# Kernel tuning notes

Measured on AMD Instinct MI355X. Metric: run time of the kernel, lower is better.

Reference implementation:

```python
import jax, jax.numpy as jnp
import numpy as np
from jax import lax

IMG_SIZE = 512
STRIDE = 16
NUM_ANCHORS = 5
NUM_CLASSES = 80
TOPK = 1000
CONF_THRESH = 0.05
NMS_THRESH = 0.6
ANCHOR_SIZE = [[32, 32], [64, 64], [128, 96], [96, 128], [256, 256]]
B = 32
FMP = IMG_SIZE // STRIDE          # 32
M = FMP * FMP * NUM_ANCHORS       # 5120


def _make_anchors():
    # mirrors YOWO.generate_anchors: grid xy (in pixels) + per-cell anchor wh
    ys, xs = jnp.meshgrid(jnp.arange(FMP), jnp.arange(FMP), indexing='ij')
    xy = jnp.stack([xs, ys], axis=-1).astype(jnp.float32).reshape(-1, 2)   # [HW,2]
    xy = jnp.repeat(xy[:, None, :], NUM_ANCHORS, axis=1) * STRIDE          # [HW,A,2]
    wh = jnp.broadcast_to(jnp.asarray(ANCHOR_SIZE, jnp.float32)[None],
                          (FMP * FMP, NUM_ANCHORS, 2))                     # [HW,A,2]
    return jnp.concatenate([xy, wh], axis=-1).reshape(-1, 4)               # [M,4]


def setup_inputs() -> dict:
    key = jax.random.key(0)
    k1, k2, k3 = jax.random.split(key, 3)
    return {
        'conf_pred': jax.random.normal(k1, (B, M, 1), jnp.float32),
        'cls_pred': jax.random.normal(k2, (B, M, NUM_CLASSES), jnp.float32),
        'reg_pred': jax.random.normal(k3, (B, M, 4), jnp.float32),
        'anchor_boxes': _make_anchors(),
    }


def _decode_bbox(anchors, reg_pred):
    # anchors/reg_pred: [..., 4] -> xyxy boxes in pixels
    xy = jax.nn.sigmoid(reg_pred[..., :2]) * STRIDE + anchors[..., :2]
    wh = jnp.exp(reg_pred[..., 2:]) * anchors[..., 2:]
    return jnp.concatenate([xy - 0.5 * wh, xy + 0.5 * wh], axis=-1)


def _pairwise_iou(boxes):
    # boxes: [K,4] xyxy -> [K,K] IoU with the exact epsilons of YOWO.nms
    x1, y1, x2, y2 = boxes[:, 0], boxes[:, 1], boxes[:, 2], boxes[:, 3]
    areas = (x2 - x1) * (y2 - y1)
    xx1 = jnp.maximum(x1[:, None], x1[None, :])
    yy1 = jnp.maximum(y1[:, None], y1[None, :])
    xx2 = jnp.minimum(x2[:, None], x2[None, :])
    yy2 = jnp.minimum(y2[:, None], y2[None, :])
    w = jnp.maximum(1e-28, xx2 - xx1)
    h = jnp.maximum(1e-28, yy2 - yy1)
    inter = w * h
    return inter / (areas[:, None] + areas[None, :] - inter + 1e-14)


def _sequential_nms_keep(iou):
    # boxes assumed sorted by descending score; greedy sequential suppression
    K = iou.shape[0]
    idx = jnp.arange(K)

    def body(i, keep):
        sup = (iou[i] > NMS_THRESH) & (idx > i) & keep[i]
        return keep & ~sup

    return lax.fori_loop(0, K, body, jnp.ones(K, bool))


def reference(conf_pred, cls_pred, reg_pred, anchor_boxes):
    # scoring: sigmoid(obj) * softmax(cls), max over classes  -> [B,M]
    score_all = jax.nn.sigmoid(conf_pred) * jax.nn.softmax(cls_pred, axis=-1)
    scores = jnp.max(score_all, axis=-1)
    labels = jnp.argmax(score_all, axis=-1)

    # topk (lax.top_k returns scores sorted descending)  -> [B,TOPK]
    scores, idx = lax.top_k(scores, TOPK)
    labels = jnp.take_along_axis(labels, idx, axis=1)
    reg_sel = jnp.take_along_axis(reg_pred, idx[..., None], axis=1)
    anc_sel = anchor_boxes[idx]                                   # [B,TOPK,4]

    bboxes = jnp.clip(_decode_bbox(anc_sel, reg_sel) / IMG_SIZE, 0.0, 1.0)

    # per-class NMS via class-offset trick (boxes in [0,1], offset 2.0 per class)
    boxes_off = bboxes + 2.0 * labels.astype(bboxes.dtype)[..., None]
    iou = jax.vmap(_pairwise_iou)(boxes_off)                      # [B,TOPK,TOPK]
    nms_keep = jax.vmap(_sequential_nms_keep)(iou)                # [B,TOPK] bool

    keep = nms_keep & (scores >= CONF_THRESH)
    scores_out = jnp.where(keep, scores, 0.0)
    return scores_out, labels, bboxes, keep
```

## Files before the change

kernel.cpp:

```cpp
#include <hip/hip_runtime.h>
#include <cstdint>
#include <math.h>

constexpr int B = 32;
constexpr int M = 5120;
constexpr int C = 80;
constexpr int K = 1000;
constexpr float NMS_T  = 0.6f;

constexpr int OFF_SCORE = 0;
constexpr int OFF_LAB   = B * K;
constexpr int OFF_BOX   = 2 * B * K;
constexpr int OFF_KEEP  = 2 * B * K + 4 * B * K;

constexpr size_t WS_KEYS     = 0;
constexpr size_t WS_LABELS   = WS_KEYS   + (size_t)B * M * 8;
constexpr size_t WS_SELIDX   = WS_LABELS + (size_t)B * M * 4;
constexpr size_t WS_SELSC    = WS_SELIDX + (size_t)B * K * 4;
constexpr size_t WS_SELLAB   = WS_SELSC + (size_t)B * K * 4;
constexpr size_t WS_BOXOFF   = WS_SELLAB + (size_t)B * K * 4;
constexpr size_t WS_MASK     = WS_BOXOFF + (size_t)B * K * 4 * 4;

__device__ __forceinline__ float expf_cr(float x) {
    return (float)exp((double)x);
}
__device__ __forceinline__ float sigm_np(float x) {
    float e = expf_cr(-x);
    return __fdiv_rn(1.0f, __fadd_rn(1.0f, e));
}

__global__ void k_scores(const float* __restrict__ conf, const float* __restrict__ cls,
                         unsigned long long* __restrict__ keys, int* __restrict__ labels) {
    int m = blockIdx.x * blockDim.x + threadIdx.x;
    int b = blockIdx.y;
    size_t t = (size_t)b * M + m;
    const float4* rowv = (const float4*)(cls + t * C);
    float ev[80];
#pragma unroll
    for (int i = 0; i < 20; i++) {
        float4 v = rowv[i];
        ev[4 * i + 0] = v.x; ev[4 * i + 1] = v.y;
        ev[4 * i + 2] = v.z; ev[4 * i + 3] = v.w;
    }
    float mx = ev[0];
#pragma unroll
    for (int c = 1; c < 80; c++) mx = fmaxf(mx, ev[c]);
#pragma unroll
    for (int c = 0; c < 80; c++) ev[c] = expf_cr(__fsub_rn(ev[c], mx));
    float r[8];
#pragma unroll
    for (int j = 0; j < 8; j++) r[j] = ev[j];
#pragma unroll
    for (int i = 8; i < 80; i += 8)
#pragma unroll
        for (int j = 0; j < 8; j++) r[j] = __fadd_rn(r[j], ev[i + j]);
    float sum = __fadd_rn(
        __fadd_rn(__fadd_rn(r[0], r[1]), __fadd_rn(r[2], r[3])),
        __fadd_rn(__fadd_rn(r[4], r[5]), __fadd_rn(r[6], r[7])));
    float s = sigm_np(conf[t]);
    float best = -1.0f; int bi = 0;
#pragma unroll
    for (int c = 0; c < 80; c++) {
        float p  = __fdiv_rn(ev[c], sum);
        float sc = __fmul_rn(s, p);
        if (sc > best) { best = sc; bi = c; }
    }
    keys[t] = ((unsigned long long)__float_as_uint(best) << 32) |
              (unsigned long long)(0xFFFFFFFFu - (unsigned)m);
    labels[t] = bi;
}

__global__ void __launch_bounds__(1024)
k_topk(const unsigned long long* __restrict__ keys,
       const int* __restrict__ labels,
       int* __restrict__ sel_idx, float* __restrict__ sel_score,
       int* __restrict__ sel_label) {
    int b = blockIdx.x;
    int tid = threadIdx.x;
    const unsigned long long* kb = keys + (size_t)b * M;

    __shared__ unsigned int hist[2048];
    __shared__ unsigned int sufA[2048];
    __shared__ unsigned int sufB[2048];
    __shared__ unsigned long long cand[2048];
    __shared__ int scnt, thrBin, ovf;

    for (int i = tid; i < 2048; i += 1024) hist[i] = 0;
    if (tid == 0) { scnt = 0; ovf = 0; }
    __syncthreads();

    unsigned long long k5[5];
#pragma unroll
    for (int i = 0; i < 5; i++) {
        k5[i] = kb[tid + i * 1024];
        atomicAdd(&hist[(unsigned)(k5[i] >> 51)], 1u);
    }
    __syncthreads();
    for (int i = tid; i < 2048; i += 1024) sufA[i] = hist[i];
    __syncthreads();
    unsigned int* src = sufA; unsigned int* dst = sufB;
    for (int d = 1; d < 2048; d <<= 1) {
        for (int i = tid; i < 2048; i += 1024) {
            unsigned int v = src[i];
            if (i + d < 2048) v += src[i + d];
            dst[i] = v;
        }
        __syncthreads();
        unsigned int* tmp = src; src = dst; dst = tmp;
    }
    for (int i = tid; i < 2048; i += 1024) {
        unsigned int s = src[i];
        unsigned int sn = (i + 1 < 2048) ? src[i + 1] : 0u;
        if (s >= (unsigned)K && sn < (unsigned)K) thrBin = i;
    }
    __syncthreads();
    int T = thrBin;
#pragma unroll
    for (int i = 0; i < 5; i++) {
        if ((int)(k5[i] >> 51) >= T) {
            int pos = atomicAdd(&scnt, 1);
            if (pos < 2048) cand[pos] = k5[i]; else ovf = 1;
        }
    }
    __syncthreads();
    if (!ovf) {
        int S = scnt;
        for (int i = tid; i < 2048; i += 1024)
            if (i >= S) cand[i] = 0ull;
        __syncthreads();
        for (int ksz = 2; ksz <= 2048; ksz <<= 1) {
            for (int jsz = ksz >> 1; jsz > 0; jsz >>= 1) {
                int i = 2 * tid - (tid & (jsz - 1));
                unsigned long long a = cand[i], c = cand[i + jsz];
                bool desc = ((i & ksz) == 0);
                if ((a < c) == desc) { cand[i] = c; cand[i + jsz] = a; }
                __syncthreads();
            }
        }
        if (tid < K) {
            unsigned long long key = cand[tid];
            unsigned int mm = 0xFFFFFFFFu - (unsigned)(key & 0xFFFFFFFFu);
            sel_idx[b * K + tid] = (int)mm;
            sel_score[b * K + tid] = __uint_as_float((unsigned)(key >> 32));
            sel_label[b * K + tid] = labels[(size_t)b * M + mm];
        }
    } else {
#pragma unroll
        for (int i = 0; i < 5; i++) {
            unsigned long long my = k5[i];
            int rank = 0;
            for (int j = 0; j < M; j++) rank += (kb[j] > my) ? 1 : 0;
            if (rank < K) {
                int mm = tid + i * 1024;
                sel_idx[b * K + rank] = mm;
                sel_score[b * K + rank] = __uint_as_float((unsigned)(my >> 32));
                sel_label[b * K + rank] = labels[(size_t)b * M + mm];
            }
        }
    }
}

__global__ void k_decode(const float* __restrict__ reg, const float* __restrict__ anchors,
                         const int* __restrict__ sel_idx, const int* __restrict__ sel_label,
                         float* __restrict__ out, float4* __restrict__ boxes_off) {
    int k = blockIdx.x * blockDim.x + threadIdx.x;
    int b = blockIdx.y;
    if (k >= K) return;
    int m = sel_idx[b * K + k];
    float4 r = ((const float4*)reg)[(size_t)b * M + m];
    float4 a = ((const float4*)anchors)[m];
    float cx = __fadd_rn(__fmul_rn(sigm_np(r.x), 16.0f), a.x);
    float cy = __fadd_rn(__fmul_rn(sigm_np(r.y), 16.0f), a.y);
    float w  = __fmul_rn(expf_cr(r.z), a.z);
    float h  = __fmul_rn(expf_cr(r.w), a.w);
    float x1 = __fdiv_rn(__fsub_rn(cx, __fmul_rn(0.5f, w)), 512.0f);
    float y1 = __fdiv_rn(__fsub_rn(cy, __fmul_rn(0.5f, h)), 512.0f);
    float x2 = __fdiv_rn(__fadd_rn(cx, __fmul_rn(0.5f, w)), 512.0f);
    float y2 = __fdiv_rn(__fadd_rn(cy, __fmul_rn(0.5f, h)), 512.0f);
    x1 = fminf(fmaxf(x1, 0.0f), 1.0f);
    y1 = fminf(fmaxf(y1, 0.0f), 1.0f);
    x2 = fminf(fmaxf(x2, 0.0f), 1.0f);
    y2 = fminf(fmaxf(y2, 0.0f), 1.0f);
    int lab = sel_label[b * K + k];
    ((float4*)(out + OFF_BOX))[b * K + k] = make_float4(x1, y1, x2, y2);
    out[OFF_LAB + b * K + k] = (float)lab;
    float off = __fmul_rn(2.0f, (float)lab);
    boxes_off[b * K + k] = make_float4(__fadd_rn(x1, off), __fadd_rn(y1, off),
                                       __fadd_rn(x2, off), __fadd_rn(y2, off));
}

__global__ void __launch_bounds__(256)
k_mask(const float4* __restrict__ boxes_off,
       unsigned long long* __restrict__ mask) {
    int b = blockIdx.z;
    int rowTile = blockIdx.x;
    int wgGroup = blockIdx.y;
    int tid = threadIdx.x;
    __shared__ float4 sbj[256];
    __shared__ float  saj[256];
    __shared__ float4 sbi[64];
    __shared__ float  sai[64];
    int j = wgGroup * 256 + tid;
    float4 bx = (j < K) ? boxes_off[b * K + j]
                        : make_float4(3e30f, 3e30f, -3e30f, -3e30f);
    sbj[tid] = bx;
    saj[tid] = __fmul_rn(__fsub_rn(bx.z, bx.x), __fsub_rn(bx.w, bx.y));
    if (tid < 64) {
        int i = rowTile * 64 + tid;
        float4 bv = (i < K) ? boxes_off[b * K + i] : make_float4(0, 0, 0, 0);
        sbi[tid] = bv;
        sai[tid] = __fmul_rn(__fsub_rn(bv.z, bv.x), __fsub_rn(bv.w, bv.y));
    }
    __syncthreads();
    int r  = tid & 63;
    int wg = tid >> 6;
    int i = rowTile * 64 + r;
    if (i >= K) return;
    float4 bi = sbi[r];
    float ai = sai[r];
    unsigned long long bits = 0ull;
    int base = wg * 64;
#pragma unroll 8
    for (int jj = 0; jj < 64; jj++) {
        float4 bj = sbj[base + jj];
        float xx1 = fmaxf(bi.x, bj.x), yy1 = fmaxf(bi.y, bj.y);
        float xx2 = fminf(bi.z, bj.z), yy2 = fminf(bi.w, bj.w);
        float ww = fmaxf(1e-28f, __fsub_rn(xx2, xx1));
        float hh = fmaxf(1e-28f, __fsub_rn(yy2, yy1));
        float inter = __fmul_rn(ww, hh);
        float denom = __fadd_rn(__fsub_rn(__fadd_rn(ai, saj[base + jj]), inter), 1e-14f);
        float iou = __fdiv_rn(inter, denom);
        if (iou > NMS_T) bits |= (1ull << jj);
    }
    mask[((size_t)b * K + i) * 16 + wgGroup * 4 + wg] = bits;
}

__global__ void __launch_bounds__(1024)
k_nms(const unsigned long long* __restrict__ mask,
      const float* __restrict__ sel_score,
      float* __restrict__ out) {
    int b = blockIdx.x;
    int j = threadIdx.x;
    int w = j >> 6;
    int jb = j & 63;
    __shared__ unsigned long long U[16], L[16];
    __shared__ int flag[2];
    unsigned long long rw[16];
    const unsigned long long* rowp = mask + ((size_t)b * K + j) * 16;
    if (j < K) {
#pragma unroll
        for (int t = 0; t < 16; t++) {
            unsigned long long bm;
            if (t < w)       bm = ~0ull;
            else if (t == w) bm = (jb == 0) ? 0ull : ((1ull << jb) - 1ull);
            else             bm = 0ull;
            rw[t] = bm ? (rowp[t] & bm) : 0ull;
        }
    } else {
#pragma unroll
        for (int t = 0; t < 16; t++) rw[t] = 0ull;
    }
    if (j < 16) { U[j] = (j < 15) ? ~0ull : ((1ull << 40) - 1); L[j] = 0ull; }
    if (j == 0) { flag[0] = 0; flag[1] = 0; }
    __syncthreads();
    for (int k = 0; k < 1025; k++) {
        unsigned long long supU = 0ull, supL = 0ull;
#pragma unroll
        for (int t = 0; t < 16; t++) {
            unsigned long long Ut = U[t], Lt = L[t];
            supU |= Lt & rw[t];
            supL |= Ut & rw[t];
        }
        bool nu = (j < K) && (supU == 0ull);
        bool nl = (j < K) && (supL == 0ull);
        __syncthreads();
        unsigned long long bu = __ballot(nu);
        unsigned long long bl = __ballot(nl);
        if (jb == 0) {
            U[w] = bu; L[w] = bl;
            if (bu != bl) flag[k & 1] = 1;
        }
        if (j == 0) flag[(k + 1) & 1] = 0;
        __syncthreads();
        if (flag[k & 1] == 0) break;
    }
    if (j < K) {
        bool kp = ((U[w] >> jb) & 1ull) != 0ull;
        float s = sel_score[b * K + j];
        kp = kp && (s >= 0.05f);
        out[OFF_SCORE + b * K + j] = kp ? s : 0.0f;
        out[OFF_KEEP + b * K + j]  = kp ? 1.0f : 0.0f;
    }
}

extern "C" void kernel_launch(void* const* d_in, const int* in_sizes, int n_in,
                              void* d_out, int out_size, void* d_ws, size_t ws_size,
                              hipStream_t stream) {
    const float* conf    = (const float*)d_in[0];
    const float* cls     = (const float*)d_in[1];
    const float* reg     = (const float*)d_in[2];
    const float* anchors = (const float*)d_in[3];
    float* out = (float*)d_out;
    char* ws = (char*)d_ws;

    unsigned long long* keys = (unsigned long long*)(ws + WS_KEYS);
    int*    labels   = (int*)(ws + WS_LABELS);
    int*    sel_idx  = (int*)(ws + WS_SELIDX);
    float*  sel_sc   = (float*)(ws + WS_SELSC);
    int*    sel_lab  = (int*)(ws + WS_SELLAB);
    float4* boxes_off = (float4*)(ws + WS_BOXOFF);
    unsigned long long* mask = (unsigned long long*)(ws + WS_MASK);

    k_scores<<<dim3(M / 256, B), 256, 0, stream>>>(conf, cls, keys, labels);
    k_topk  <<<B, 1024, 0, stream>>>(keys, labels, sel_idx, sel_sc, sel_lab);
    k_decode<<<dim3(4, B), 256, 0, stream>>>(reg, anchors, sel_idx, sel_lab, out, boxes_off);
    k_mask  <<<dim3(16, 4, B), 256, 0, stream>>>(boxes_off, mask);
    k_nms   <<<32, 1024, 0, stream>>>(mask, sel_sc, out);
}
```

Baseline: 165.6 us.

## Fuse decode into top-k, shrink bitonic sort, compute only lower-triangle mask tiles

Moves bbox decode into the top-k kernel, which removes one launch and the sel_idx/sel_label round trip through global memory. The bitonic sort runs over 1024 elements instead of 2048 when the candidate count allows. The IoU mask kernel now skips tiles above the diagonal, since NMS only reads lower-triangular bits, and the NMS kernel loads each mask row with 128-bit vector loads. Mask words that are never written stay uninitialised, but the NMS kernel masks them out, so correctness depends on that masking.

New measurement: 163.2 us. No clear change (-1.4%).

```diff
diff --git a/kernel.cpp b/kernel.cpp
--- a/kernel.cpp
+++ b/kernel.cpp
@@ -15,10 +15,8 @@
 
 constexpr size_t WS_KEYS     = 0;
 constexpr size_t WS_LABELS   = WS_KEYS   + (size_t)B * M * 8;
-constexpr size_t WS_SELIDX   = WS_LABELS + (size_t)B * M * 4;
-constexpr size_t WS_SELSC    = WS_SELIDX + (size_t)B * K * 4;
-constexpr size_t WS_SELLAB   = WS_SELSC + (size_t)B * K * 4;
-constexpr size_t WS_BOXOFF   = WS_SELLAB + (size_t)B * K * 4;
+constexpr size_t WS_SELSC    = WS_LABELS + (size_t)B * M * 4;
+constexpr size_t WS_BOXOFF   = WS_SELSC + (size_t)B * K * 4;
 constexpr size_t WS_MASK     = WS_BOXOFF + (size_t)B * K * 4 * 4;
 
 __device__ __forceinline__ float expf_cr(float x) {
@@ -70,103 +68,12 @@
     labels[t] = bi;
 }
 
-__global__ void __launch_bounds__(1024)
-k_topk(const unsigned long long* __restrict__ keys,
-       const int* __restrict__ labels,
-       int* __restrict__ sel_idx, float* __restrict__ sel_score,
-       int* __restrict__ sel_label) {
-    int b = blockIdx.x;
-    int tid = threadIdx.x;
-    const unsigned long long* kb = keys + (size_t)b * M;
-
-    __shared__ unsigned int hist[2048];
-    __shared__ unsigned int sufA[2048];
-    __shared__ unsigned int sufB[2048];
-    __shared__ unsigned long long cand[2048];
-    __shared__ int scnt, thrBin, ovf;
-
-    for (int i = tid; i < 2048; i += 1024) hist[i] = 0;
-    if (tid == 0) { scnt = 0; ovf = 0; }
-    __syncthreads();
-
-    unsigned long long k5[5];
-#pragma unroll
-    for (int i = 0; i < 5; i++) {
-        k5[i] = kb[tid + i * 1024];
-        atomicAdd(&hist[(unsigned)(k5[i] >> 51)], 1u);
-    }
-    __syncthreads();
-    for (int i = tid; i < 2048; i += 1024) sufA[i] = hist[i];
-    __syncthreads();
-    unsigned int* src = sufA; unsigned int* dst = sufB;
-    for (int d = 1; d < 2048; d <<= 1) {
-        for (int i = tid; i < 2048; i += 1024) {
-            unsigned int v = src[i];
-            if (i + d < 2048) v += src[i + d];
-            dst[i] = v;
-        }
-        __syncthreads();
-        unsigned int* tmp = src; src = dst; dst = tmp;
-    }
-    for (int i = tid; i < 2048; i += 1024) {
-        unsigned int s = src[i];
-        unsigned int sn = (i + 1 < 2048) ? src[i + 1] : 0u;
-        if (s >= (unsigned)K && sn < (unsigned)K) thrBin = i;
-    }
-    __syncthreads();
-    int T = thrBin;
-#pragma unroll
-    for (int i = 0; i < 5; i++) {
-        if ((int)(k5[i] >> 51) >= T) {
-            int pos = atomicAdd(&scnt, 1);
-            if (pos < 2048) cand[pos] = k5[i]; else ovf = 1;
-        }
-    }
-    __syncthreads();
-    if (!ovf) {
-        int S = scnt;
-        for (int i = tid; i < 2048; i += 1024)
-            if (i >= S) cand[i] = 0ull;
-        __syncthreads();
-        for (int ksz = 2; ksz <= 2048; ksz <<= 1) {
-            for (int jsz = ksz >> 1; jsz > 0; jsz >>= 1) {
-                int i = 2 * tid - (tid & (jsz - 1));
-                unsigned long long a = cand[i], c = cand[i + jsz];
-                bool desc = ((i & ksz) == 0);
-                if ((a < c) == desc) { cand[i] = c; cand[i + jsz] = a; }
-                __syncthreads();
-            }
-        }
-        if (tid < K) {
-            unsigned long long key = cand[tid];
-            unsigned int mm = 0xFFFFFFFFu - (unsigned)(key & 0xFFFFFFFFu);
-            sel_idx[b * K + tid] = (int)mm;
-            sel_score[b * K + tid] = __uint_as_float((unsigned)(key >> 32));
-            sel_label[b * K + tid] = labels[(size_t)b * M + mm];
-        }
-    } else {
-#pragma unroll
-        for (int i = 0; i < 5; i++) {
-            unsigned long long my = k5[i];
-            int rank = 0;
-            for (int j = 0; j < M; j++) rank += (kb[j] > my) ? 1 : 0;
-            if (rank < K) {
-                int mm = tid + i * 1024;
-                sel_idx[b * K + rank] = mm;
-                sel_score[b * K + rank] = __uint_as_float((unsigned)(my >> 32));
-                sel_label[b * K + rank] = labels[(size_t)b * M + mm];
-            }
-        }
-    }
-}
-
-__global__ void k_decode(const float* __restrict__ reg, const float* __restrict__ anchors,
-                         const int* __restrict__ sel_idx, const int* __restrict__ sel_label,
-                         float* __restrict__ out, float4* __restrict__ boxes_off) {
-    int k = blockIdx.x * blockDim.x + threadIdx.x;
-    int b = blockIdx.y;
-    if (k >= K) return;
-    int m = sel_idx[b * K + k];
+__device__ __forceinline__ void decode_write(
+    int b, int rank, int m, float score, int lab,
+    const float* __restrict__ reg, const float* __restrict__ anchors,
+    float* __restrict__ out, float4* __restrict__ boxes_off,
+    float* __restrict__ sel_score)
+{
     float4 r = ((const float4*)reg)[(size_t)b * M + m];
     float4 a = ((const float4*)anchors)[m];
     float cx = __fadd_rn(__fmul_rn(sigm_np(r.x), 16.0f), a.x);
@@ -181,12 +88,106 @@
     y1 = fminf(fmaxf(y1, 0.0f), 1.0f);
     x2 = fminf(fmaxf(x2, 0.0f), 1.0f);
     y2 = fminf(fmaxf(y2, 0.0f), 1.0f);
-    int lab = sel_label[b * K + k];
-    ((float4*)(out + OFF_BOX))[b * K + k] = make_float4(x1, y1, x2, y2);
-    out[OFF_LAB + b * K + k] = (float)lab;
+    ((float4*)(out + OFF_BOX))[b * K + rank] = make_float4(x1, y1, x2, y2);
+    out[OFF_LAB + b * K + rank] = (float)lab;
     float off = __fmul_rn(2.0f, (float)lab);
-    boxes_off[b * K + k] = make_float4(__fadd_rn(x1, off), __fadd_rn(y1, off),
-                                       __fadd_rn(x2, off), __fadd_rn(y2, off));
+    boxes_off[b * K + rank] = make_float4(__fadd_rn(x1, off), __fadd_rn(y1, off),
+                                          __fadd_rn(x2, off), __fadd_rn(y2, off));
+    sel_score[b * K + rank] = score;
+}
+
+__global__ void __launch_bounds__(1024)
+k_topk(const unsigned long long* __restrict__ keys,
+       const int* __restrict__ labels,
+       const float* __restrict__ reg, const float* __restrict__ anchors,
+       float* __restrict__ out, float4* __restrict__ boxes_off,
+       float* __restrict__ sel_score) {
+    int b = blockIdx.x;
+    int tid = threadIdx.x;
+    const unsigned long long* kb = keys + (size_t)b * M;
+
+    __shared__ unsigned int hist[2048];
+    __shared__ unsigned int sufA[2048];
+    __shared__ unsigned int sufB[2048];
+    __shared__ unsigned long long cand[2048];
+    __shared__ int scnt, thrBin, ovf;
+
+    for (int i = tid; i < 2048; i += 1024) hist[i] = 0;
+    if (tid == 0) { scnt = 0; ovf = 0; }
+    __syncthreads();
+
+    unsigned long long k5[5];
+#pragma unroll
+    for (int i = 0; i < 5; i++) {
+        k5[i] = kb[tid + i * 1024];
+        atomicAdd(&hist[(unsigned)(k5[i] >> 51)], 1u);
+    }
+    __syncthreads();
+    for (int i = tid; i < 2048; i += 1024) sufA[i] = hist[i];
+    __syncthreads();
+    unsigned int* src = sufA; unsigned int* dst = sufB;
+    for (int d = 1; d < 2048; d <<= 1) {
+        for (int i = tid; i < 2048; i += 1024) {
+            unsigned int v = src[i];
+            if (i + d < 2048) v += src[i + d];
+            dst[i] = v;
+        }
+        __syncthreads();
+        unsigned int* tmp = src; src = dst; dst = tmp;
+    }
+    for (int i = tid; i < 2048; i += 1024) {
+        unsigned int s = src[i];
+        unsigned int sn = (i + 1 < 2048) ? src[i + 1] : 0u;
+        if (s >= (unsigned)K && sn < (unsigned)K) thrBin = i;
+    }
+    __syncthreads();
+    int T = thrBin;
+#pragma unroll
+    for (int i = 0; i < 5; i++) {
+        if ((int)(k5[i] >> 51) >= T) {
+            int pos = atomicAdd(&scnt, 1);
+            if (pos < 2048) cand[pos] = k5[i]; else ovf = 1;
+        }
+    }
+    __syncthreads();
+    if (!ovf) {
+        int S = scnt;
+        int N = (S <= 1024) ? 1024 : 2048;
+        for (int i = tid; i < 2048; i += 1024)
+            if (i >= S) cand[i] = 0ull;
+        __syncthreads();
+        for (int ksz = 2; ksz <= N; ksz <<= 1) {
+            for (int jsz = ksz >> 1; jsz > 0; jsz >>= 1) {
+                if (tid < (N >> 1)) {
+                    int i = 2 * tid - (tid & (jsz - 1));
+                    unsigned long long a = cand[i], c = cand[i + jsz];
+                    bool desc = ((i & ksz) == 0);
+                    if ((a < c) == desc) { cand[i] = c; cand[i + jsz] = a; }
+                }
+                __syncthreads();
+            }
+        }
+        if (tid < K) {
+            unsigned long long key = cand[tid];
+            int mm = (int)(0xFFFFFFFFu - (unsigned)(key & 0xFFFFFFFFu));
+            float sc = __uint_as_float((unsigned)(key >> 32));
+            int lab = labels[(size_t)b * M + mm];
+            decode_write(b, tid, mm, sc, lab, reg, anchors, out, boxes_off, sel_score);
+        }
+    } else {
+#pragma unroll
+        for (int i = 0; i < 5; i++) {
+            unsigned long long my = k5[i];
+            int rank = 0;
+            for (int j = 0; j < M; j++) rank += (kb[j] > my) ? 1 : 0;
+            if (rank < K) {
+                int mm = tid + i * 1024;
+                float sc = __uint_as_float((unsigned)(my >> 32));
+                int lab = labels[(size_t)b * M + mm];
+                decode_write(b, rank, mm, sc, lab, reg, anchors, out, boxes_off, sel_score);
+            }
+        }
+    }
 }
 
 __global__ void __launch_bounds__(256)
@@ -195,6 +196,7 @@
     int b = blockIdx.z;
     int rowTile = blockIdx.x;
     int wgGroup = blockIdx.y;
+    if (4 * wgGroup > rowTile) return;
     int tid = threadIdx.x;
     __shared__ float4 sbj[256];
     __shared__ float  saj[256];
@@ -214,6 +216,8 @@
     __syncthreads();
     int r  = tid & 63;
     int wg = tid >> 6;
+    int W  = wgGroup * 4 + wg;
+    if (W > rowTile) return;
     int i = rowTile * 64 + r;
     if (i >= K) return;
     float4 bi = sbi[r];
@@ -232,7 +236,7 @@
         float iou = __fdiv_rn(inter, denom);
         if (iou > NMS_T) bits |= (1ull << jj);
     }
-    mask[((size_t)b * K + i) * 16 + wgGroup * 4 + wg] = bits;
+    mask[((size_t)b * K + i) * 16 + W] = bits;
 }
 
 __global__ void __launch_bounds__(1024)
@@ -246,15 +250,20 @@
     __shared__ unsigned long long U[16], L[16];
     __shared__ int flag[2];
     unsigned long long rw[16];
-    const unsigned long long* rowp = mask + ((size_t)b * K + j) * 16;
     if (j < K) {
+        const ulonglong2* rp2 =
+            (const ulonglong2*)(mask + ((size_t)b * K + j) * 16);
+#pragma unroll
+        for (int t = 0; t < 8; t++) {
+            ulonglong2 v = rp2[t];
+            rw[2 * t] = v.x; rw[2 * t + 1] = v.y;
+        }
 #pragma unroll
         for (int t = 0; t < 16; t++) {
-            unsigned long long bm;
-            if (t < w)       bm = ~0ull;
-            else if (t == w) bm = (jb == 0) ? 0ull : ((1ull << jb) - 1ull);
-            else             bm = 0ull;
-            rw[t] = bm ? (rowp[t] & bm) : 0ull;
+            unsigned long long bm =
+                (t < w) ? ~0ull
+                        : ((t == w && jb != 0) ? ((1ull << jb) - 1ull) : 0ull);
+            rw[t] &= bm;
         }
     } else {
 #pragma unroll
@@ -305,15 +314,12 @@
 
     unsigned long long* keys = (unsigned long long*)(ws + WS_KEYS);
     int*    labels   = (int*)(ws + WS_LABELS);
-    int*    sel_idx  = (int*)(ws + WS_SELIDX);
     float*  sel_sc   = (float*)(ws + WS_SELSC);
-    int*    sel_lab  = (int*)(ws + WS_SELLAB);
     float4* boxes_off = (float4*)(ws + WS_BOXOFF);
     unsigned long long* mask = (unsigned long long*)(ws + WS_MASK);
 
     k_scores<<<dim3(M / 256, B), 256, 0, stream>>>(conf, cls, keys, labels);
-    k_topk  <<<B, 1024, 0, stream>>>(keys, labels, sel_idx, sel_sc, sel_lab);
-    k_decode<<<dim3(4, B), 256, 0, stream>>>(reg, anchors, sel_idx, sel_lab, out, boxes_off);
+    k_topk  <<<B, 1024, 0, stream>>>(keys, labels, reg, anchors, out, boxes_off, sel_sc);
     k_mask  <<<dim3(16, 4, B), 256, 0, stream>>>(boxes_off, mask);
     k_nms   <<<32, 1024, 0, stream>>>(mask, sel_sc, out);
 }
```
